# Kernel tuning notes

Hardware: AMD Instinct MI355X
Metric: run time of the kernel (lower is better)

Reference implementation:

```python
import jax, jax.numpy as jnp
import numpy as np

EPS = 1e-8  # torch CosineSimilarity default eps

def _cossim(a, b):
    # a, b: [B, C, n]; cosine similarity over channel dim C
    dot = jnp.sum(a * b, axis=1)
    na = jnp.linalg.norm(a, axis=1)
    nb = jnp.linalg.norm(b, axis=1)
    return dot / jnp.maximum(na * nb, EPS)

def setup_inputs() -> dict:
    key = jax.random.key(0)
    k1, k2, k3, k4 = jax.random.split(key, 4)
    B, C, W, H = 4, 256, 256, 256
    n = W  # reduction = 1
    x1 = jax.random.normal(k1, (B, C, W, H), dtype=jnp.float32)
    x2 = jax.random.normal(k2, (B, C, W, H), dtype=jnp.float32)
    rand_int1 = jax.random.randint(k3, (n,), 0, W * H, dtype=jnp.int64 if jax.config.jax_enable_x64 else jnp.int32)
    rand_int2 = jax.random.randint(k4, (n,), 0, W * H, dtype=jnp.int64 if jax.config.jax_enable_x64 else jnp.int32)
    return {"x1": x1, "x2": x2, "rand_int1": rand_int1, "rand_int2": rand_int2}

def reference(x1, x2, rand_int1, rand_int2):
    B, C, W, H = x1.shape
    x1f = x1.reshape(B, C, W * H)
    x2f = x2.reshape(B, C, W * H)
    # Fused gather over all n sampled pixel pairs: [B, C, n]
    a1 = x1f[:, :, rand_int1]
    b1 = x1f[:, :, rand_int2]
    a2 = x2f[:, :, rand_int1]
    b2 = x2f[:, :, rand_int2]
    D1 = _cossim(a1, b1)  # [B, n]
    D2 = _cossim(a2, b2)  # [B, n]
    # mode == 'unchange'
    return jnp.mean(jnp.abs(D1 - D2))
```

## Files before the change

### kernel.cpp

```cpp
#include <hip/hip_runtime.h>
#include <hip/hip_bf16.h>
#include <math.h>

#define BDIM 4
#define CDIM 256
#define WH   65536
#define NIDX 256

__inline__ __device__ float wave_reduce_sum(float v) {
    #pragma unroll
    for (int off = 32; off > 0; off >>= 1)
        v += __shfl_down(v, off, 64);
    return v;
}

__global__ __launch_bounds__(256) void cossim_pairs_kernel(
        const float* __restrict__ x1, const float* __restrict__ x2,
        const int* __restrict__ i1, const int* __restrict__ i2,
        float* __restrict__ partial) {
    const int blk = blockIdx.x;
    const int b   = blk >> 8;
    const int j   = blk & (NIDX - 1);
    const int c   = threadIdx.x;

    const int idx1 = i1[j];
    const int idx2 = i2[j];

    const size_t base = ((size_t)b * CDIM + c) * (size_t)WH;

    const float a1 = __builtin_nontemporal_load(&x1[base + (size_t)idx1]);
    const float b1 = __builtin_nontemporal_load(&x1[base + (size_t)idx2]);
    const float a2 = __builtin_nontemporal_load(&x2[base + (size_t)idx1]);
    const float b2 = __builtin_nontemporal_load(&x2[base + (size_t)idx2]);

    float s[6];
    s[0] = a1 * b1;
    s[1] = a1 * a1;
    s[2] = b1 * b1;
    s[3] = a2 * b2;
    s[4] = a2 * a2;
    s[5] = b2 * b2;

    __shared__ float sm[4][6];
    const int lane = c & 63;
    const int wid  = c >> 6;
    #pragma unroll
    for (int k = 0; k < 6; ++k) {
        float r = wave_reduce_sum(s[k]);
        if (lane == 0) sm[wid][k] = r;
    }
    __syncthreads();

    if (c == 0) {
        float t[6];
        #pragma unroll
        for (int k = 0; k < 6; ++k)
            t[k] = sm[0][k] + sm[1][k] + sm[2][k] + sm[3][k];
        const float denom1 = fmaxf(sqrtf(t[1]) * sqrtf(t[2]), 1e-8f);
        const float denom2 = fmaxf(sqrtf(t[4]) * sqrtf(t[5]), 1e-8f);
        const float D1 = t[0] / denom1;
        const float D2 = t[3] / denom2;
        partial[blk] = fabsf(D1 - D2);
    }
}

__global__ __launch_bounds__(256) void final_mean_kernel(
        const float* __restrict__ partial, float* __restrict__ out) {
    const int t = threadIdx.x;
    float v = partial[t] + partial[t + 256] + partial[t + 512] + partial[t + 768];
    v = wave_reduce_sum(v);
    __shared__ float sm[4];
    if ((t & 63) == 0) sm[t >> 6] = v;
    __syncthreads();
    if (t == 0)
        out[0] = (sm[0] + sm[1] + sm[2] + sm[3]) * (1.0f / (float)(BDIM * NIDX));
}

extern "C" void kernel_launch(void* const* d_in, const int* in_sizes, int n_in,
                              void* d_out, int out_size, void* d_ws, size_t ws_size,
                              hipStream_t stream) {
    const float* x1 = (const float*)d_in[0];
    const float* x2 = (const float*)d_in[1];
    const int*   i1 = (const int*)d_in[2];
    const int*   i2 = (const int*)d_in[3];
    float* out = (float*)d_out;
    float* partial = (float*)d_ws;

    const int nblocks = BDIM * NIDX;
    cossim_pairs_kernel<<<nblocks, 256, 0, stream>>>(x1, x2, i1, i2, partial);
    final_mean_kernel<<<1, 256, 0, stream>>>(partial, out);
}
```

Baseline: 30.03 us.

## Sort gather indices and gather per channel row before reducing in second pass

Adds a bitonic sort of the 512 sampled pixel indices so each block gathers one channel row in sorted address order, which should improve locality within each 256KB plane. Products are written to an 8-float-strided workspace, and a second kernel reduces over channels per pair. This trades the original single-pass gather, whose per-thread loads were 256KB apart, for two extra kernel launches and about 8MB of intermediate writes and reads.

```diff
diff --git a/kernel.cpp b/kernel.cpp
--- a/kernel.cpp
+++ b/kernel.cpp
@@ -6,6 +6,8 @@
 #define CDIM 256
 #define WH   65536
 #define NIDX 256
+#define NPOS 512
+#define WSTR 8
 
 __inline__ __device__ float wave_reduce_sum(float v) {
     #pragma unroll
@@ -14,32 +16,88 @@
     return v;
 }
 
-__global__ __launch_bounds__(256) void cossim_pairs_kernel(
+__global__ __launch_bounds__(256) void sort_idx_kernel(
+        const int* __restrict__ i1, const int* __restrict__ i2,
+        unsigned int* __restrict__ sorted) {
+    __shared__ unsigned int key[NPOS];
+    const int t = threadIdx.x;
+    key[t]       = ((unsigned int)i1[t] << 16) | (unsigned int)t;
+    key[t + 256] = ((unsigned int)i2[t] << 16) | (unsigned int)(t + 256);
+    __syncthreads();
+    for (int k = 2; k <= NPOS; k <<= 1) {
+        for (int jj = k >> 1; jj > 0; jj >>= 1) {
+            #pragma unroll
+            for (int i0 = 0; i0 < 2; ++i0) {
+                const int i = t + (i0 << 8);
+                const int l = i ^ jj;
+                if (l > i) {
+                    const unsigned int a = key[i], b = key[l];
+                    const bool asc = ((i & k) == 0);
+                    if ((a > b) == asc) { key[i] = b; key[l] = a; }
+                }
+            }
+            __syncthreads();
+        }
+    }
+    sorted[t] = key[t];
+    sorted[t + 256] = key[t + 256];
+}
+
+__global__ __launch_bounds__(256) void gather_pass1(
         const float* __restrict__ x1, const float* __restrict__ x2,
-        const int* __restrict__ i1, const int* __restrict__ i2,
-        float* __restrict__ partial) {
+        const unsigned int* __restrict__ sorted,
+        float* __restrict__ prod) {
     const int blk = blockIdx.x;
     const int b   = blk >> 8;
-    const int j   = blk & (NIDX - 1);
+    const int c   = blk & 255;
+    const int t   = threadIdx.x;
+
+    __shared__ unsigned int skey[NPOS];
+    __shared__ float v1[NPOS], v2[NPOS];
+    skey[t]       = sorted[t];
+    skey[t + 256] = sorted[t + 256];
+    __syncthreads();
+
+    const size_t base = ((size_t)(b * CDIM + c)) * (size_t)WH;
+
+    const unsigned int k0 = skey[t];
+    const unsigned int k1 = skey[t + 256];
+    const unsigned int p0 = k0 >> 16, s0 = k0 & 0xFFFFu;
+    const unsigned int p1 = k1 >> 16, s1 = k1 & 0xFFFFu;
+
+    const float a0 = x1[base + p0];
+    const float a1 = x1[base + p1];
+    const float g0 = x2[base + p0];
+    const float g1 = x2[base + p1];
+
+    v1[s0] = a0; v1[s1] = a1;
+    v2[s0] = g0; v2[s1] = g1;
+    __syncthreads();
+
+    const float A1 = v1[t], B1 = v1[t + 256];
+    const float A2 = v2[t], B2 = v2[t + 256];
+
+    float* w = prod + (((((size_t)b << 8) | t) << 8) + c) * WSTR;
+    float4 w0, w1;
+    w0.x = A1 * B1; w0.y = A1 * A1; w0.z = B1 * B1; w0.w = A2 * B2;
+    w1.x = A2 * A2; w1.y = B2 * B2; w1.z = 0.0f;    w1.w = 0.0f;
+    *(float4*)(w)     = w0;
+    *(float4*)(w + 4) = w1;
+}
+
+__global__ __launch_bounds__(256) void reduce_pass2(
+        const float* __restrict__ prod, float* __restrict__ partial) {
+    const int blk = blockIdx.x;
+    const int b   = blk >> 8;
+    const int j   = blk & 255;
     const int c   = threadIdx.x;
 
-    const int idx1 = i1[j];
-    const int idx2 = i2[j];
+    const float4* p = (const float4*)(prod +
+        (((((size_t)b << 8) | j) << 8) + c) * WSTR);
+    const float4 u = p[0];
+    const float4 v = p[1];
 
-    const size_t base = ((size_t)b * CDIM + c) * (size_t)WH;
-
-    const float a1 = __builtin_nontemporal_load(&x1[base + (size_t)idx1]);
-    const float b1 = __builtin_nontemporal_load(&x1[base + (size_t)idx2]);
-    const float a2 = __builtin_nontemporal_load(&x2[base + (size_t)idx1]);
-    const float b2 = __builtin_nontemporal_load(&x2[base + (size_t)idx2]);
-
-    float s[6];
-    s[0] = a1 * b1;
-    s[1] = a1 * a1;
-    s[2] = b1 * b1;
-    s[3] = a2 * b2;
-    s[4] = a2 * a2;
-    s[5] = b2 * b2;
+    float s[6] = { u.x, u.y, u.z, u.w, v.x, v.y };
 
     __shared__ float sm[4][6];
     const int lane = c & 63;
@@ -58,9 +116,7 @@
             t[k] = sm[0][k] + sm[1][k] + sm[2][k] + sm[3][k];
         const float denom1 = fmaxf(sqrtf(t[1]) * sqrtf(t[2]), 1e-8f);
         const float denom2 = fmaxf(sqrtf(t[4]) * sqrtf(t[5]), 1e-8f);
-        const float D1 = t[0] / denom1;
-        const float D2 = t[3] / denom2;
-        partial[blk] = fabsf(D1 - D2);
+        partial[blk] = fabsf(t[0] / denom1 - t[3] / denom2);
     }
 }
 
@@ -84,9 +140,13 @@
     const int*   i1 = (const int*)d_in[2];
     const int*   i2 = (const int*)d_in[3];
     float* out = (float*)d_out;
-    float* partial = (float*)d_ws;
 
-    const int nblocks = BDIM * NIDX;
-    cossim_pairs_kernel<<<nblocks, 256, 0, stream>>>(x1, x2, i1, i2, partial);
+    unsigned int* sorted = (unsigned int*)d_ws;
+    float* partial = (float*)((char*)d_ws + 4096);
+    float* prod    = (float*)((char*)d_ws + 8192);
+
+    sort_idx_kernel<<<1, 256, 0, stream>>>(i1, i2, sorted);
+    gather_pass1<<<BDIM * CDIM, 256, 0, stream>>>(x1, x2, sorted, prod);
+    reduce_pass2<<<BDIM * NIDX, 256, 0, stream>>>(prod, partial);
     final_mean_kernel<<<1, 256, 0, stream>>>(partial, out);
 }
```

Result: slower. 42.51 us (+41.6%).
